# Kernel tuning notes

Hardware: AMD Instinct MI355X
Metric: run time of the kernel (lower is better)

Reference implementation:

```python
import jax, jax.numpy as jnp
import numpy as np

H = 1024      # hidden_size
NH = 8        # num_attention_heads
HD = H // NH  # head dim = 128
FF = 3072     # DebertaConfig default intermediate_size
MAXPOS = 512  # max_position_embeddings
EPS = 1e-7    # DeBERTa layer_norm_eps


def layer_norm(x, g, b):
    m = jnp.mean(x, axis=-1, keepdims=True)
    v = jnp.mean((x - m) ** 2, axis=-1, keepdims=True)
    return (x - m) * jax.lax.rsqrt(v + EPS) * g + b


def setup_inputs() -> dict:
    key = jax.random.key(0)
    ks = jax.random.split(key, 12)
    s = 0.02  # init std
    B, S = 16, 512
    return {
        "x": jax.random.normal(ks[0], (B, S, H), jnp.float32),
        "pos_emb": jax.random.normal(ks[1], (MAXPOS, H), jnp.float32) * s,
        "emb_ln_g": jnp.ones((H,), jnp.float32),
        "emb_ln_b": jnp.zeros((H,), jnp.float32),
        "Wq": jax.random.normal(ks[2], (H, H), jnp.float32) * s,
        "Wk": jax.random.normal(ks[3], (H, H), jnp.float32) * s,
        "Wv": jax.random.normal(ks[4], (H, H), jnp.float32) * s,
        "q_bias": jax.random.normal(ks[5], (H,), jnp.float32) * s,
        "v_bias": jax.random.normal(ks[6], (H,), jnp.float32) * s,
        "Wo": jax.random.normal(ks[7], (H, H), jnp.float32) * s,
        "bo": jnp.zeros((H,), jnp.float32),
        "ln1_g": jnp.ones((H,), jnp.float32),
        "ln1_b": jnp.zeros((H,), jnp.float32),
        "Wi": jax.random.normal(ks[8], (H, FF), jnp.float32) * s,
        "bi": jnp.zeros((FF,), jnp.float32),
        "Wf": jax.random.normal(ks[9], (FF, H), jnp.float32) * s,
        "bf": jnp.zeros((H,), jnp.float32),
        "ln2_g": jnp.ones((H,), jnp.float32),
        "ln2_b": jnp.zeros((H,), jnp.float32),
    }


def reference(x, pos_emb, emb_ln_g, emb_ln_b, Wq, Wk, Wv, q_bias, v_bias,
              Wo, bo, ln1_g, ln1_b, Wi, bi, Wf, bf, ln2_g, ln2_b):
    B, S, _ = x.shape
    # DebertaEmbeddings: inputs_embeds + absolute position embeddings, LayerNorm (eval: no dropout)
    h = layer_norm(x + pos_emb[:S], emb_ln_g, emb_ln_b)
    # DisentangledSelfAttention with pos_att_type=[] -> standard attention, scale_factor=1;
    # in_proj has no bias, but q and v get learned bias vectors.
    q = (h @ Wq + q_bias).reshape(B, S, NH, HD).transpose(0, 2, 1, 3)  # [B,NH,S,HD]
    k = (h @ Wk).reshape(B, S, NH, HD).transpose(0, 2, 1, 3)
    v = (h @ Wv + v_bias).reshape(B, S, NH, HD).transpose(0, 2, 1, 3)
    scale = jnp.sqrt(jnp.asarray(HD, x.dtype))
    scores = jnp.einsum('bhqd,bhkd->bhqk', q / scale, k)  # [B,NH,S,S]
    probs = jax.nn.softmax(scores, axis=-1)  # attention_mask all ones -> plain softmax
    ctx = jnp.einsum('bhqk,bhkd->bhqd', probs, v)
    ctx = ctx.transpose(0, 2, 1, 3).reshape(B, S, H)
    # SelfOutput: dense + residual + LayerNorm
    attn_out = layer_norm(ctx @ Wo + bo + h, ln1_g, ln1_b)
    # Intermediate (exact gelu) + Output: dense + residual + LayerNorm
    ff = jax.nn.gelu(attn_out @ Wi + bi, approximate=False)
    out = layer_norm(ff @ Wf + bf + attn_out, ln2_g, ln2_b)
    return out
```

## Files before the change

kernel.cpp:

```cpp
#include <hip/hip_runtime.h>
#include <hip/hip_bf16.h>

#define BB  16
#define SS  512
#define HH  1024
#define NHH 8
#define HDD 128
#define FFF 3072
#define TT  (BB * SS)

typedef __hip_bfloat16 bf16;
typedef short s8v __attribute__((ext_vector_type(8)));
typedef float f4v __attribute__((ext_vector_type(4)));

__device__ __forceinline__ float bf2f(bf16 v) { return __bfloat162float(v); }
__device__ __forceinline__ bf16 f2bf(float f) { return __float2bfloat16(f); }
__device__ __forceinline__ float us2f(unsigned short u) {
  union { unsigned int i; float f; } c; c.i = (unsigned int)u << 16; return c.f;
}

__global__ void embed_ln_kernel(const float* __restrict__ x, const float* __restrict__ pos,
                                const float* __restrict__ g, const float* __restrict__ bta,
                                bf16* __restrict__ h) {
  int t = blockIdx.x;
  int s = t & (SS - 1);
  int tid = threadIdx.x;
  const float* xr = x + (size_t)t * HH;
  const float* pr = pos + (size_t)s * HH;
  float vals[4];
  float sum = 0.f;
#pragma unroll
  for (int i = 0; i < 4; i++) {
    int c = tid + i * 256;
    vals[i] = xr[c] + pr[c];
    sum += vals[i];
  }
  __shared__ float red[4];
#pragma unroll
  for (int off = 32; off > 0; off >>= 1) sum += __shfl_down(sum, off, 64);
  if ((tid & 63) == 0) red[tid >> 6] = sum;
  __syncthreads();
  float mean = (red[0] + red[1] + red[2] + red[3]) * (1.f / HH);
  float vsum = 0.f;
#pragma unroll
  for (int i = 0; i < 4; i++) { float d = vals[i] - mean; vsum += d * d; }
  __syncthreads();
#pragma unroll
  for (int off = 32; off > 0; off >>= 1) vsum += __shfl_down(vsum, off, 64);
  if ((tid & 63) == 0) red[tid >> 6] = vsum;
  __syncthreads();
  float rstd = rsqrtf((red[0] + red[1] + red[2] + red[3]) * (1.f / HH) + 1e-7f);
  bf16* hr = h + (size_t)t * HH;
#pragma unroll
  for (int i = 0; i < 4; i++) {
    int c = tid + i * 256;
    hr[c] = f2bf((vals[i] - mean) * rstd * g[c] + bta[c]);
  }
}

template <int OUT_F32>
__global__ void add_ln_kernel(const bf16* __restrict__ a, const bf16* __restrict__ res,
                              const float* __restrict__ g, const float* __restrict__ bta,
                              void* __restrict__ outv) {
  int t = blockIdx.x;
  int tid = threadIdx.x;
  const bf16* ar = a + (size_t)t * HH;
  const bf16* rr = res + (size_t)t * HH;
  float vals[4];
  float sum = 0.f;
#pragma unroll
  for (int i = 0; i < 4; i++) {
    int c = tid + i * 256;
    vals[i] = bf2f(ar[c]) + bf2f(rr[c]);
    sum += vals[i];
  }
  __shared__ float red[4];
#pragma unroll
  for (int off = 32; off > 0; off >>= 1) sum += __shfl_down(sum, off, 64);
  if ((tid & 63) == 0) red[tid >> 6] = sum;
  __syncthreads();
  float mean = (red[0] + red[1] + red[2] + red[3]) * (1.f / HH);
  float vsum = 0.f;
#pragma unroll
  for (int i = 0; i < 4; i++) { float d = vals[i] - mean; vsum += d * d; }
  __syncthreads();
#pragma unroll
  for (int off = 32; off > 0; off >>= 1) vsum += __shfl_down(vsum, off, 64);
  if ((tid & 63) == 0) red[tid >> 6] = vsum;
  __syncthreads();
  float rstd = rsqrtf((red[0] + red[1] + red[2] + red[3]) * (1.f / HH) + 1e-7f);
#pragma unroll
  for (int i = 0; i < 4; i++) {
    int c = tid + i * 256;
    float o = (vals[i] - mean) * rstd * g[c] + bta[c];
    if (OUT_F32)
      ((float*)outv)[(size_t)t * HH + c] = o;
    else
      ((bf16*)outv)[(size_t)t * HH + c] = f2bf(o);
  }
}

__global__ void convert_w_kernel(const float* __restrict__ W, bf16* __restrict__ Wt,
                                 int K, int N) {
  __shared__ float tile[32][33];
  int n0 = blockIdx.x * 32, k0 = blockIdx.y * 32;
#pragma unroll
  for (int it = 0; it < 4; it++) {
    int idx = threadIdx.x + it * 256;
    int ty = idx >> 5, tx = idx & 31;
    tile[ty][tx] = W[(size_t)(k0 + ty) * N + n0 + tx];
  }
  __syncthreads();
#pragma unroll
  for (int it = 0; it < 4; it++) {
    int idx = threadIdx.x + it * 256;
    int ty = idx >> 5, tx = idx & 31;
    Wt[(size_t)(n0 + ty) * K + k0 + tx] = f2bf(tile[tx][ty]);
  }
}

__global__ void build_qkv_bias_kernel(const float* __restrict__ qb,
                                      const float* __restrict__ vb,
                                      float* __restrict__ o) {
  int i = blockIdx.x * 256 + threadIdx.x;
  float v = 0.f;
  if (i < HH) v = qb[i];
  else if (i >= 2 * HH) v = vb[i - 2 * HH];
  o[i] = v;
}

__global__ void transpose_v_kernel(const bf16* __restrict__ v, bf16* __restrict__ vt) {
  __shared__ unsigned short tile[32][33];
  int bh = blockIdx.z;
  int s0 = blockIdx.x * 32, d0 = blockIdx.y * 32;
  int b = bh >> 3, hd = bh & 7;
  const unsigned short* vp = (const unsigned short*)v + ((size_t)b * SS) * (3 * HH) + hd * HDD;
  unsigned short* vtp = (unsigned short*)vt + (size_t)bh * HDD * SS;
#pragma unroll
  for (int it = 0; it < 4; it++) {
    int idx = threadIdx.x + it * 256;
    int ty = idx >> 5, tx = idx & 31;
    tile[ty][tx] = vp[(size_t)(s0 + ty) * (3 * HH) + d0 + tx];
  }
  __syncthreads();
#pragma unroll
  for (int it = 0; it < 4; it++) {
    int idx = threadIdx.x + it * 256;
    int ty = idx >> 5, tx = idx & 31;
    vtp[(size_t)(d0 + ty) * SS + s0 + tx] = tile[tx][ty];
  }
}

template <int GELU>
__global__ __launch_bounds__(256)
void mfma_gemm_kernel(const bf16* __restrict__ A, int lda, long long sAb, long long sAh,
                      const bf16* __restrict__ Bt, int ldb, long long sBb, long long sBh,
                      const float* __restrict__ bias,
                      bf16* __restrict__ C, int ldc, long long sCb, long long sCh,
                      int M, int N, int K, float scale) {
  __shared__ unsigned short Als[128 * 40];
  __shared__ unsigned short Bls[128 * 40];
  int tid = threadIdx.x;
  int lane = tid & 63, wave = tid >> 6;
  int l15 = lane & 15, quad = lane >> 4;
  int wm = wave & 1, wn = wave >> 1;
  int m0 = blockIdx.y * 128, n0 = blockIdx.x * 128;
  int zb = blockIdx.z >> 3, zh = blockIdx.z & 7;
  const bf16* Ab = A + zb * sAb + zh * sAh;
  const bf16* Bb = Bt + zb * sBb + zh * sBh;
  bf16* Cb = C + zb * sCb + zh * sCh;
  f4v acc[4][4];
#pragma unroll
  for (int i = 0; i < 4; i++)
#pragma unroll
    for (int j = 0; j < 4; j++) acc[i][j] = (f4v){0.f, 0.f, 0.f, 0.f};
  int r0 = tid >> 2;
  int q8 = (tid & 3) * 8;
  const bf16* Ap0 = Ab + (size_t)(m0 + r0) * lda + q8;
  const bf16* Ap1 = Ab + (size_t)(m0 + r0 + 64) * lda + q8;
  const bf16* Bp0 = Bb + (size_t)(n0 + r0) * ldb + q8;
  const bf16* Bp1 = Bb + (size_t)(n0 + r0 + 64) * ldb + q8;
  uint4 a0 = *(const uint4*)(Ap0);
  uint4 a1 = *(const uint4*)(Ap1);
  uint4 b0 = *(const uint4*)(Bp0);
  uint4 b1 = *(const uint4*)(Bp1);
  for (int k0 = 0; k0 < K; k0 += 32) {
    *(uint4*)&Als[r0 * 40 + q8] = a0;
    *(uint4*)&Als[(r0 + 64) * 40 + q8] = a1;
    *(uint4*)&Bls[r0 * 40 + q8] = b0;
    *(uint4*)&Bls[(r0 + 64) * 40 + q8] = b1;
    __syncthreads();
    int kn = k0 + 32;
    if (kn < K) {
      a0 = *(const uint4*)(Ap0 + kn);
      a1 = *(const uint4*)(Ap1 + kn);
      b0 = *(const uint4*)(Bp0 + kn);
      b1 = *(const uint4*)(Bp1 + kn);
    }
    s8v af[4], bfr[4];
#pragma unroll
    for (int i = 0; i < 4; i++)
      af[i] = *(const s8v*)&Als[(wm * 64 + i * 16 + l15) * 40 + quad * 8];
#pragma unroll
    for (int j = 0; j < 4; j++)
      bfr[j] = *(const s8v*)&Bls[(wn * 64 + j * 16 + l15) * 40 + quad * 8];
#pragma unroll
    for (int i = 0; i < 4; i++)
#pragma unroll
      for (int j = 0; j < 4; j++)
        acc[i][j] = __builtin_amdgcn_mfma_f32_16x16x32_bf16(af[i], bfr[j], acc[i][j], 0, 0, 0);
    __syncthreads();
  }
#pragma unroll
  for (int i = 0; i < 4; i++) {
#pragma unroll
    for (int j = 0; j < 4; j++) {
      int n = n0 + wn * 64 + j * 16 + l15;
      float bval = bias ? bias[n] : 0.f;
#pragma unroll
      for (int r = 0; r < 4; r++) {
        int m = m0 + wm * 64 + i * 16 + quad * 4 + r;
        float v = (acc[i][j][r] + bval) * scale;
        if (GELU) v = 0.5f * v * (1.f + erff(v * 0.70710678118654752f));
        Cb[(size_t)m * ldc + n] = f2bf(v);
      }
    }
  }
}

__global__ void softmax_kernel(bf16* __restrict__ sc) {
  int wave = threadIdx.x >> 6, lane = threadIdx.x & 63;
  size_t row = (size_t)blockIdx.x * 4 + wave;
  unsigned short* p = (unsigned short*)sc + row * SS + lane * 8;
  union { uint4 u4; unsigned short u[8]; } buf;
  buf.u4 = *(const uint4*)p;
  float v[8];
  float mx = -1e30f;
#pragma unroll
  for (int j = 0; j < 8; j++) { v[j] = us2f(buf.u[j]); mx = fmaxf(mx, v[j]); }
#pragma unroll
  for (int off = 32; off > 0; off >>= 1) mx = fmaxf(mx, __shfl_xor(mx, off));
  float sum = 0.f;
#pragma unroll
  for (int j = 0; j < 8; j++) { v[j] = __expf(v[j] - mx); sum += v[j]; }
#pragma unroll
  for (int off = 32; off > 0; off >>= 1) sum += __shfl_xor(sum, off);
  float inv = 1.f / sum;
  union { uint4 u4; unsigned short u[8]; } obuf;
#pragma unroll
  for (int j = 0; j < 8; j++) {
    bf16 b = f2bf(v[j] * inv);
    obuf.u[j] = *(unsigned short*)&b;
  }
  *(uint4*)p = obuf.u4;
}

extern "C" void kernel_launch(void* const* d_in, const int* in_sizes, int n_in,
                              void* d_out, int out_size, void* d_ws, size_t ws_size,
                              hipStream_t stream) {
  const float* x     = (const float*)d_in[0];
  const float* pos   = (const float*)d_in[1];
  const float* eg    = (const float*)d_in[2];
  const float* ebeta = (const float*)d_in[3];
  const float* Wq    = (const float*)d_in[4];
  const float* Wk    = (const float*)d_in[5];
  const float* Wv    = (const float*)d_in[6];
  const float* qbias = (const float*)d_in[7];
  const float* vbias = (const float*)d_in[8];
  const float* Wo    = (const float*)d_in[9];
  const float* bo    = (const float*)d_in[10];
  const float* l1g   = (const float*)d_in[11];
  const float* l1b   = (const float*)d_in[12];
  const float* Wi    = (const float*)d_in[13];
  const float* bi    = (const float*)d_in[14];
  const float* Wf    = (const float*)d_in[15];
  const float* bfb   = (const float*)d_in[16];
  const float* l2g   = (const float*)d_in[17];
  const float* l2b   = (const float*)d_in[18];

  char* w = (char*)d_ws;
  const size_t MB = (size_t)1 << 20;
  bf16* h      = (bf16*)(w + 0 * MB);
  bf16* qkv    = (bf16*)(w + 16 * MB);
  bf16* ctx    = (bf16*)(w + 64 * MB);
  bf16* tmp1   = (bf16*)(w + 80 * MB);
  bf16* attn   = (bf16*)(w + 96 * MB);
  bf16* scores = (bf16*)(w + 112 * MB);
  bf16* ff     = (bf16*)(w + 112 * MB);
  bf16* tmp2   = (bf16*)(w + 176 * MB);
  bf16* vt     = (bf16*)(w + 192 * MB);
  bf16* Wqkvt  = (bf16*)(w + 208 * MB);
  bf16* Wot    = (bf16*)(w + 214 * MB);
  bf16* Wit    = (bf16*)(w + 216 * MB);
  bf16* Wft    = (bf16*)(w + 222 * MB);
  float* qkvb  = (float*)(w + 228 * MB);
  float* out   = (float*)d_out;

  const float QSCALE = 0.08838834764831845f;

  embed_ln_kernel<<<TT, 256, 0, stream>>>(x, pos, eg, ebeta, h);

  convert_w_kernel<<<dim3(HH / 32, HH / 32), 256, 0, stream>>>(Wq, Wqkvt, HH, HH);
  convert_w_kernel<<<dim3(HH / 32, HH / 32), 256, 0, stream>>>(Wk, Wqkvt + (size_t)HH * HH, HH, HH);
  convert_w_kernel<<<dim3(HH / 32, HH / 32), 256, 0, stream>>>(Wv, Wqkvt + (size_t)2 * HH * HH, HH, HH);
  convert_w_kernel<<<dim3(HH / 32, HH / 32), 256, 0, stream>>>(Wo, Wot, HH, HH);
  convert_w_kernel<<<dim3(FFF / 32, HH / 32), 256, 0, stream>>>(Wi, Wit, HH, FFF);
  convert_w_kernel<<<dim3(HH / 32, FFF / 32), 256, 0, stream>>>(Wf, Wft, FFF, HH);
  build_qkv_bias_kernel<<<12, 256, 0, stream>>>(qbias, vbias, qkvb);

  mfma_gemm_kernel<0><<<dim3(24, 64, 1), 256, 0, stream>>>(
      h, HH, 0, 0, Wqkvt, HH, 0, 0, qkvb, qkv, 3 * HH, 0, 0, TT, 3 * HH, HH, 1.f);

  mfma_gemm_kernel<0><<<dim3(4, 4, BB * NHH), 256, 0, stream>>>(
      qkv, 3 * HH, (long long)SS * 3 * HH, HDD,
      qkv + HH, 3 * HH, (long long)SS * 3 * HH, HDD,
      nullptr,
      scores, SS, (long long)NHH * SS * SS, (long long)SS * SS,
      SS, SS, HDD, QSCALE);

  softmax_kernel<<<BB * NHH * SS / 4, 256, 0, stream>>>(scores);

  transpose_v_kernel<<<dim3(SS / 32, HDD / 32, BB * NHH), 256, 0, stream>>>(qkv + 2 * HH, vt);

  mfma_gemm_kernel<0><<<dim3(1, 4, BB * NHH), 256, 0, stream>>>(
      scores, SS, (long long)NHH * SS * SS, (long long)SS * SS,
      vt, SS, (long long)NHH * HDD * SS, (long long)HDD * SS,
      nullptr,
      ctx, HH, (long long)SS * HH, HDD,
      SS, HDD, SS, 1.f);

  mfma_gemm_kernel<0><<<dim3(8, 64, 1), 256, 0, stream>>>(
      ctx, HH, 0, 0, Wot, HH, 0, 0, bo, tmp1, HH, 0, 0, TT, HH, HH, 1.f);
  add_ln_kernel<0><<<TT, 256, 0, stream>>>(tmp1, h, l1g, l1b, attn);

  mfma_gemm_kernel<1><<<dim3(24, 64, 1), 256, 0, stream>>>(
      attn, HH, 0, 0, Wit, HH, 0, 0, bi, ff, FFF, 0, 0, TT, FFF, HH, 1.f);
  mfma_gemm_kernel<0><<<dim3(8, 64, 1), 256, 0, stream>>>(
      ff, FFF, 0, 0, Wft, FFF, 0, 0, bfb, tmp2, HH, 0, 0, TT, HH, FFF, 1.f);
  add_ln_kernel<1><<<TT, 256, 0, stream>>>(tmp2, attn, l2g, l2b, out);
}
```

Measured before the change: 531.8 us.

## Add 256x256-tile MFMA GEMM with direct global-to-LDS staging for dense projections

Introduces a new 512-thread GEMM kernel using 256x256 output tiles, double-buffered LDS filled via global_load_lds with XOR-swizzled layout, interleaved with 16x16x32 bf16 MFMAs under raised wave priority. It replaces the previous 128x128-style GEMM for the QKV, output, intermediate and final FFN projections. The aim is higher arithmetic intensity per block and overlap of global loads with MFMA work. In exchange it uses 128KB LDS per block and many registers, which limits occupancy, and it relies on hand-placed barriers and vmcnt waits whose correctness depends on exact load counts.

```diff
diff --git a/kernel.cpp b/kernel.cpp
--- a/kernel.cpp
+++ b/kernel.cpp
@@ -228,6 +228,177 @@
   }
 }
 
+#define G256_BAR() asm volatile("s_barrier" ::: "memory")
+
+__device__ __forceinline__ void g256_stage_half(
+    const bf16* __restrict__ base, int ldx, int tile, int half,
+    unsigned op_byte, unsigned short* lds, int trow, int tcol8, int wave) {
+  const bf16* g0 = base + (size_t)(half * 128 + trow) * ldx + tile * 64 + tcol8;
+  const bf16* g1 = g0 + (size_t)64 * ldx;
+  unsigned off = op_byte + (unsigned)(tile & 1) * 32768u + (unsigned)half * 16384u +
+                 (unsigned)wave * 1024u;
+  unsigned l0 = (unsigned)(size_t)((char*)lds + off);
+  unsigned l1 = l0 + 8192u;
+  __builtin_amdgcn_global_load_lds(
+      (const __attribute__((address_space(1))) void*)(size_t)g0,
+      (__attribute__((address_space(3))) unsigned int*)l0, 16, 0, 0);
+  __builtin_amdgcn_global_load_lds(
+      (const __attribute__((address_space(1))) void*)(size_t)g1,
+      (__attribute__((address_space(3))) unsigned int*)l1, 16, 0, 0);
+}
+
+__device__ __forceinline__ void g256_read_a(
+    const unsigned short* lds, int buf, int sel, int wm, int l15, int quad,
+    s8v out[4][2]) {
+  int xr = l15 & 7;
+#pragma unroll
+  for (int i = 0; i < 4; i++) {
+    int R = wm * 128 + sel * 64 + i * 16 + l15;
+#pragma unroll
+    for (int kk = 0; kk < 2; kk++) {
+      int ch = (kk * 4 + quad) ^ xr;
+      out[i][kk] = *(const s8v*)&lds[buf * 16384 + R * 64 + ch * 8];
+    }
+  }
+}
+
+__device__ __forceinline__ void g256_read_b(
+    const unsigned short* lds, int buf, int sel, int wn, int l15, int quad,
+    s8v out[2][2]) {
+  int xr = l15 & 7;
+#pragma unroll
+  for (int j = 0; j < 2; j++) {
+    int R = wn * 64 + sel * 32 + j * 16 + l15;
+#pragma unroll
+    for (int kk = 0; kk < 2; kk++) {
+      int ch = (kk * 4 + quad) ^ xr;
+      out[j][kk] = *(const s8v*)&lds[32768 + buf * 16384 + R * 64 + ch * 8];
+    }
+  }
+}
+
+__device__ __forceinline__ void g256_mfma_quad(
+    const s8v a[4][2], const s8v b[2][2], f4v acc[8][4], int ag, int bg) {
+  __builtin_amdgcn_s_setprio(1);
+#pragma unroll
+  for (int i = 0; i < 4; i++)
+#pragma unroll
+    for (int j = 0; j < 2; j++)
+#pragma unroll
+      for (int kk = 0; kk < 2; kk++)
+        acc[ag * 4 + i][bg * 2 + j] = __builtin_amdgcn_mfma_f32_16x16x32_bf16(
+            a[i][kk], b[j][kk], acc[ag * 4 + i][bg * 2 + j], 0, 0, 0);
+  __builtin_amdgcn_s_setprio(0);
+}
+
+template <int GELU>
+__global__ __launch_bounds__(512, 2)
+void gemm256_kernel(const bf16* __restrict__ A, int lda,
+                    const bf16* __restrict__ Bt, int ldb,
+                    const float* __restrict__ bias,
+                    bf16* __restrict__ C, int ldc,
+                    int M, int N, int K) {
+  __shared__ __align__(128) unsigned short lds[65536];
+  int tid = threadIdx.x;
+  int lane = tid & 63, wave = tid >> 6;
+  int l15 = lane & 15, quad = lane >> 4;
+  int wm = wave >> 2, wn = wave & 3;
+  int m0 = blockIdx.y * 256, n0 = blockIdx.x * 256;
+  int trow = tid >> 3;
+  int tcol8 = ((tid & 7) ^ ((tid >> 3) & 7)) * 8;
+  const bf16* Ag = A + (size_t)m0 * lda;
+  const bf16* Bg = Bt + (size_t)n0 * ldb;
+
+  f4v acc[8][4];
+#pragma unroll
+  for (int i = 0; i < 8; i++)
+#pragma unroll
+    for (int j = 0; j < 4; j++) acc[i][j] = (f4v){0.f, 0.f, 0.f, 0.f};
+
+  g256_stage_half(Ag, lda, 0, 0, 0, lds, trow, tcol8, wave);
+  g256_stage_half(Ag, lda, 0, 1, 0, lds, trow, tcol8, wave);
+  g256_stage_half(Bg, ldb, 0, 0, 65536, lds, trow, tcol8, wave);
+  g256_stage_half(Bg, ldb, 0, 1, 65536, lds, trow, tcol8, wave);
+  g256_stage_half(Ag, lda, 1, 0, 0, lds, trow, tcol8, wave);
+  g256_stage_half(Ag, lda, 1, 1, 0, lds, trow, tcol8, wave);
+  g256_stage_half(Bg, ldb, 1, 0, 65536, lds, trow, tcol8, wave);
+  asm volatile("s_waitcnt vmcnt(6)" ::: "memory");
+  G256_BAR();
+
+  int niter = K >> 7;
+  for (int it = 0; it < niter; ++it) {
+    int t = it * 2;
+    bool more = (it < niter - 1);
+    s8v a0[4][2], a1[4][2], b0f[2][2], b1f[2][2];
+    g256_read_a(lds, 0, 0, wm, l15, quad, a0);
+    g256_read_b(lds, 0, 0, wn, l15, quad, b0f);
+    g256_stage_half(Bg, ldb, t + 1, 1, 65536, lds, trow, tcol8, wave);
+    G256_BAR();
+    g256_mfma_quad(a0, b0f, acc, 0, 0);
+    G256_BAR();
+    g256_read_a(lds, 0, 1, wm, l15, quad, a1);
+    g256_read_b(lds, 0, 1, wn, l15, quad, b1f);
+    G256_BAR();
+    g256_mfma_quad(a1, b0f, acc, 1, 0);
+    G256_BAR();
+    if (more) {
+      g256_stage_half(Ag, lda, t + 2, 0, 0, lds, trow, tcol8, wave);
+      g256_stage_half(Ag, lda, t + 2, 1, 0, lds, trow, tcol8, wave);
+    }
+    G256_BAR();
+    g256_mfma_quad(a1, b1f, acc, 1, 1);
+    G256_BAR();
+    if (more) g256_stage_half(Bg, ldb, t + 2, 0, 65536, lds, trow, tcol8, wave);
+    G256_BAR();
+    g256_mfma_quad(a0, b1f, acc, 0, 1);
+    if (more) { asm volatile("s_waitcnt vmcnt(6)" ::: "memory"); }
+    else      { asm volatile("s_waitcnt vmcnt(0)" ::: "memory"); }
+    G256_BAR();
+    g256_read_a(lds, 1, 0, wm, l15, quad, a0);
+    g256_read_b(lds, 1, 0, wn, l15, quad, b0f);
+    if (more) g256_stage_half(Bg, ldb, t + 2, 1, 65536, lds, trow, tcol8, wave);
+    G256_BAR();
+    g256_mfma_quad(a0, b0f, acc, 0, 0);
+    G256_BAR();
+    g256_read_a(lds, 1, 1, wm, l15, quad, a1);
+    g256_read_b(lds, 1, 1, wn, l15, quad, b1f);
+    G256_BAR();
+    g256_mfma_quad(a1, b0f, acc, 1, 0);
+    G256_BAR();
+    if (more) {
+      g256_stage_half(Ag, lda, t + 3, 0, 0, lds, trow, tcol8, wave);
+      g256_stage_half(Ag, lda, t + 3, 1, 0, lds, trow, tcol8, wave);
+    }
+    G256_BAR();
+    g256_mfma_quad(a1, b1f, acc, 1, 1);
+    G256_BAR();
+    if (more) g256_stage_half(Bg, ldb, t + 3, 0, 65536, lds, trow, tcol8, wave);
+    G256_BAR();
+    g256_mfma_quad(a0, b1f, acc, 0, 1);
+    if (more) asm volatile("s_waitcnt vmcnt(6)" ::: "memory");
+    G256_BAR();
+  }
+
+#pragma unroll
+  for (int sa = 0; sa < 2; sa++)
+#pragma unroll
+    for (int i = 0; i < 4; i++)
+#pragma unroll
+      for (int sb = 0; sb < 2; sb++)
+#pragma unroll
+        for (int j = 0; j < 2; j++) {
+          int n = n0 + wn * 64 + sb * 32 + j * 16 + l15;
+          float bval = bias[n];
+#pragma unroll
+          for (int r = 0; r < 4; r++) {
+            int m = m0 + wm * 128 + sa * 64 + i * 16 + quad * 4 + r;
+            float v = acc[sa * 4 + i][sb * 2 + j][r] + bval;
+            if (GELU) v = 0.5f * v * (1.f + erff(v * 0.70710678118654752f));
+            C[(size_t)m * ldc + n] = f2bf(v);
+          }
+        }
+}
+
 __global__ void softmax_kernel(bf16* __restrict__ sc) {
   int wave = threadIdx.x >> 6, lane = threadIdx.x & 63;
   size_t row = (size_t)blockIdx.x * 4 + wave;
@@ -308,8 +479,8 @@
   convert_w_kernel<<<dim3(HH / 32, FFF / 32), 256, 0, stream>>>(Wf, Wft, FFF, HH);
   build_qkv_bias_kernel<<<12, 256, 0, stream>>>(qbias, vbias, qkvb);
 
-  mfma_gemm_kernel<0><<<dim3(24, 64, 1), 256, 0, stream>>>(
-      h, HH, 0, 0, Wqkvt, HH, 0, 0, qkvb, qkv, 3 * HH, 0, 0, TT, 3 * HH, HH, 1.f);
+  gemm256_kernel<0><<<dim3(12, 32), 512, 0, stream>>>(
+      h, HH, Wqkvt, HH, qkvb, qkv, 3 * HH, TT, 3 * HH, HH);
 
   mfma_gemm_kernel<0><<<dim3(4, 4, BB * NHH), 256, 0, stream>>>(
       qkv, 3 * HH, (long long)SS * 3 * HH, HDD,
@@ -329,13 +500,13 @@
       ctx, HH, (long long)SS * HH, HDD,
       SS, HDD, SS, 1.f);
 
-  mfma_gemm_kernel<0><<<dim3(8, 64, 1), 256, 0, stream>>>(
-      ctx, HH, 0, 0, Wot, HH, 0, 0, bo, tmp1, HH, 0, 0, TT, HH, HH, 1.f);
+  gemm256_kernel<0><<<dim3(4, 32), 512, 0, stream>>>(
+      ctx, HH, Wot, HH, bo, tmp1, HH, TT, HH, HH);
   add_ln_kernel<0><<<TT, 256, 0, stream>>>(tmp1, h, l1g, l1b, attn);
 
-  mfma_gemm_kernel<1><<<dim3(24, 64, 1), 256, 0, stream>>>(
-      attn, HH, 0, 0, Wit, HH, 0, 0, bi, ff, FFF, 0, 0, TT, FFF, HH, 1.f);
-  mfma_gemm_kernel<0><<<dim3(8, 64, 1), 256, 0, stream>>>(
-      ff, FFF, 0, 0, Wft, FFF, 0, 0, bfb, tmp2, HH, 0, 0, TT, HH, FFF, 1.f);
+  gemm256_kernel<1><<<dim3(12, 32), 512, 0, stream>>>(
+      attn, HH, Wit, HH, bi, ff, FFF, TT, FFF, HH);
+  gemm256_kernel<0><<<dim3(4, 32), 512, 0, stream>>>(
+      ff, FFF, Wft, FFF, bfb, tmp2, HH, TT, HH, FFF);
   add_ln_kernel<1><<<TT, 256, 0, stream>>>(tmp2, attn, l2g, l2b, out);
 }
```

Result: slower. 694.1 us (+30.5%).

## Load GEMM tiles directly into LDS with XOR-swizzled layout

Applied to the files above, without the earlier changes.

The MFMA GEMM now copies A and B tiles straight from global memory into LDS using global_load_lds, instead of going through registers. The LDS tile shrinks from padded rows of 40 to unpadded rows of 32. An XOR swizzle on the 8-element column chunks is meant to avoid bank conflicts on the fragment reads. This frees the registers used for staging, but it drops the register prefetch of the next K slice, so global load latency is no longer overlapped with the MFMA work inside a block.

```diff
diff --git a/kernel.cpp b/kernel.cpp
--- a/kernel.cpp
+++ b/kernel.cpp
@@ -158,8 +158,8 @@
                       const float* __restrict__ bias,
                       bf16* __restrict__ C, int ldc, long long sCb, long long sCh,
                       int M, int N, int K, float scale) {
-  __shared__ unsigned short Als[128 * 40];
-  __shared__ unsigned short Bls[128 * 40];
+  __shared__ __align__(16) unsigned short Als[128 * 32];
+  __shared__ __align__(16) unsigned short Bls[128 * 32];
   int tid = threadIdx.x;
   int lane = tid & 63, wave = tid >> 6;
   int l15 = lane & 15, quad = lane >> 4;
@@ -174,36 +174,43 @@
   for (int i = 0; i < 4; i++)
 #pragma unroll
     for (int j = 0; j < 4; j++) acc[i][j] = (f4v){0.f, 0.f, 0.f, 0.f};
-  int r0 = tid >> 2;
-  int q8 = (tid & 3) * 8;
-  const bf16* Ap0 = Ab + (size_t)(m0 + r0) * lda + q8;
-  const bf16* Ap1 = Ab + (size_t)(m0 + r0 + 64) * lda + q8;
-  const bf16* Bp0 = Bb + (size_t)(n0 + r0) * ldb + q8;
-  const bf16* Bp1 = Bb + (size_t)(n0 + r0 + 64) * ldb + q8;
-  uint4 a0 = *(const uint4*)(Ap0);
-  uint4 a1 = *(const uint4*)(Ap1);
-  uint4 b0 = *(const uint4*)(Bp0);
-  uint4 b1 = *(const uint4*)(Bp1);
+
+  int srow = tid >> 2;
+  int scol = ((tid & 3) ^ (srow & 3)) * 8;
+  const bf16* ApLo = Ab + (size_t)(m0 + srow) * lda + scol;
+  const bf16* ApHi = Ab + (size_t)(m0 + srow + 64) * lda + scol;
+  const bf16* BpLo = Bb + (size_t)(n0 + srow) * ldb + scol;
+  const bf16* BpHi = Bb + (size_t)(n0 + srow + 64) * ldb + scol;
+  unsigned lA0 = (unsigned)(size_t)(Als + tid * 8);
+  unsigned lA1 = (unsigned)(size_t)(Als + 2048 + tid * 8);
+  unsigned lB0 = (unsigned)(size_t)(Bls + tid * 8);
+  unsigned lB1 = (unsigned)(size_t)(Bls + 2048 + tid * 8);
+
   for (int k0 = 0; k0 < K; k0 += 32) {
-    *(uint4*)&Als[r0 * 40 + q8] = a0;
-    *(uint4*)&Als[(r0 + 64) * 40 + q8] = a1;
-    *(uint4*)&Bls[r0 * 40 + q8] = b0;
-    *(uint4*)&Bls[(r0 + 64) * 40 + q8] = b1;
+    __builtin_amdgcn_global_load_lds(
+        (const __attribute__((address_space(1))) void*)(ApLo + k0),
+        (__attribute__((address_space(3))) unsigned int*)(size_t)lA0, 16, 0, 0);
+    __builtin_amdgcn_global_load_lds(
+        (const __attribute__((address_space(1))) void*)(ApHi + k0),
+        (__attribute__((address_space(3))) unsigned int*)(size_t)lA1, 16, 0, 0);
+    __builtin_amdgcn_global_load_lds(
+        (const __attribute__((address_space(1))) void*)(BpLo + k0),
+        (__attribute__((address_space(3))) unsigned int*)(size_t)lB0, 16, 0, 0);
+    __builtin_amdgcn_global_load_lds(
+        (const __attribute__((address_space(1))) void*)(BpHi + k0),
+        (__attribute__((address_space(3))) unsigned int*)(size_t)lB1, 16, 0, 0);
     __syncthreads();
-    int kn = k0 + 32;
-    if (kn < K) {
-      a0 = *(const uint4*)(Ap0 + kn);
-      a1 = *(const uint4*)(Ap1 + kn);
-      b0 = *(const uint4*)(Bp0 + kn);
-      b1 = *(const uint4*)(Bp1 + kn);
+    s8v af[4], bfr[4];
+#pragma unroll
+    for (int i = 0; i < 4; i++) {
+      int R = wm * 64 + i * 16 + l15;
+      af[i] = *(const s8v*)&Als[R * 32 + ((quad ^ (R & 3)) * 8)];
     }
-    s8v af[4], bfr[4];
-#pragma unroll
-    for (int i = 0; i < 4; i++)
-      af[i] = *(const s8v*)&Als[(wm * 64 + i * 16 + l15) * 40 + quad * 8];
-#pragma unroll
-    for (int j = 0; j < 4; j++)
-      bfr[j] = *(const s8v*)&Bls[(wn * 64 + j * 16 + l15) * 40 + quad * 8];
+#pragma unroll
+    for (int j = 0; j < 4; j++) {
+      int R = wn * 64 + j * 16 + l15;
+      bfr[j] = *(const s8v*)&Bls[R * 32 + ((quad ^ (R & 3)) * 8)];
+    }
 #pragma unroll
     for (int i = 0; i < 4; i++)
 #pragma unroll
```

After: 566.2 us. +6.5%, slower.

## Swizzle GEMM LDS layout and add double-buffered direct-to-LDS GEMM for FFN up-projection

Applied to the files above, without the earlier changes.

Replaces the padded 40-element LDS row stride with a 32-element stride plus an XOR swizzle on the 16-byte chunk index, which avoids bank conflicts while using less shared memory in every GEMM. It also adds a new GEMM kernel for the GELU intermediate projection. That kernel uses global_load_lds to stream tiles straight into double-buffered LDS, so the next tile's loads overlap the current tile's MFMAs. In exchange the code depends on the LDS-direct load semantics and the XOR layout matching the per-lane write ordering, and it relies on only one barrier per iteration for correctness.

```diff
diff --git a/kernel.cpp b/kernel.cpp
--- a/kernel.cpp
+++ b/kernel.cpp
@@ -158,8 +158,8 @@
                       const float* __restrict__ bias,
                       bf16* __restrict__ C, int ldc, long long sCb, long long sCh,
                       int M, int N, int K, float scale) {
-  __shared__ unsigned short Als[128 * 40];
-  __shared__ unsigned short Bls[128 * 40];
+  __shared__ __align__(16) unsigned short Als[128 * 32];
+  __shared__ __align__(16) unsigned short Bls[128 * 32];
   int tid = threadIdx.x;
   int lane = tid & 63, wave = tid >> 6;
   int l15 = lane & 15, quad = lane >> 4;
@@ -176,6 +176,10 @@
     for (int j = 0; j < 4; j++) acc[i][j] = (f4v){0.f, 0.f, 0.f, 0.f};
   int r0 = tid >> 2;
   int q8 = (tid & 3) * 8;
+  int fw = (r0 >> 1) & 3;
+  int wlo = r0 * 32 + (((tid & 3) ^ fw) * 8);
+  int whi = (r0 + 64) * 32 + (((tid & 3) ^ fw) * 8);
+  int qx = (quad ^ ((l15 >> 1) & 3)) * 8;
   const bf16* Ap0 = Ab + (size_t)(m0 + r0) * lda + q8;
   const bf16* Ap1 = Ab + (size_t)(m0 + r0 + 64) * lda + q8;
   const bf16* Bp0 = Bb + (size_t)(n0 + r0) * ldb + q8;
@@ -185,10 +189,10 @@
   uint4 b0 = *(const uint4*)(Bp0);
   uint4 b1 = *(const uint4*)(Bp1);
   for (int k0 = 0; k0 < K; k0 += 32) {
-    *(uint4*)&Als[r0 * 40 + q8] = a0;
-    *(uint4*)&Als[(r0 + 64) * 40 + q8] = a1;
-    *(uint4*)&Bls[r0 * 40 + q8] = b0;
-    *(uint4*)&Bls[(r0 + 64) * 40 + q8] = b1;
+    *(uint4*)&Als[wlo] = a0;
+    *(uint4*)&Als[whi] = a1;
+    *(uint4*)&Bls[wlo] = b0;
+    *(uint4*)&Bls[whi] = b1;
     __syncthreads();
     int kn = k0 + 32;
     if (kn < K) {
@@ -200,10 +204,10 @@
     s8v af[4], bfr[4];
 #pragma unroll
     for (int i = 0; i < 4; i++)
-      af[i] = *(const s8v*)&Als[(wm * 64 + i * 16 + l15) * 40 + quad * 8];
+      af[i] = *(const s8v*)&Als[(wm * 64 + i * 16 + l15) * 32 + qx];
 #pragma unroll
     for (int j = 0; j < 4; j++)
-      bfr[j] = *(const s8v*)&Bls[(wn * 64 + j * 16 + l15) * 40 + quad * 8];
+      bfr[j] = *(const s8v*)&Bls[(wn * 64 + j * 16 + l15) * 32 + qx];
 #pragma unroll
     for (int i = 0; i < 4; i++)
 #pragma unroll
@@ -223,6 +227,90 @@
         float v = (acc[i][j][r] + bval) * scale;
         if (GELU) v = 0.5f * v * (1.f + erff(v * 0.70710678118654752f));
         Cb[(size_t)m * ldc + n] = f2bf(v);
+      }
+    }
+  }
+}
+
+template <int GELU>
+__global__ __launch_bounds__(256)
+void gemm_dbuf_kernel(const bf16* __restrict__ A, int lda,
+                      const bf16* __restrict__ Bt, int ldb,
+                      const float* __restrict__ bias,
+                      bf16* __restrict__ C, int ldc,
+                      int M, int N, int K, float scale) {
+  __shared__ __align__(16) unsigned short As2[2 * 128 * 32];
+  __shared__ __align__(16) unsigned short Bs2[2 * 128 * 32];
+  int tid = threadIdx.x;
+  int lane = tid & 63, wave = tid >> 6;
+  int l15 = lane & 15, quad = lane >> 4;
+  int wm = wave & 1, wn = wave >> 1;
+  int m0 = blockIdx.y * 128, n0 = blockIdx.x * 128;
+  f4v acc[4][4];
+#pragma unroll
+  for (int i = 0; i < 4; i++)
+#pragma unroll
+    for (int j = 0; j < 4; j++) acc[i][j] = (f4v){0.f, 0.f, 0.f, 0.f};
+  int srow = tid >> 2;
+  int scol = (((tid & 3) ^ ((tid >> 3) & 3))) * 8;
+  const bf16* ApLo = A + (size_t)(m0 + srow) * lda + scol;
+  const bf16* ApHi = A + (size_t)(m0 + srow + 64) * lda + scol;
+  const bf16* BpLo = Bt + (size_t)(n0 + srow) * ldb + scol;
+  const bf16* BpHi = Bt + (size_t)(n0 + srow + 64) * ldb + scol;
+  int qx = (quad ^ ((l15 >> 1) & 3)) * 8;
+  int niter = K >> 5;
+
+#define V2_STAGE(kk, buf) do {                                                  \
+    unsigned _o = (unsigned)(buf) * 4096u + (unsigned)tid * 8u;                 \
+    __builtin_amdgcn_global_load_lds(                                           \
+        (const __attribute__((address_space(1))) void*)(ApLo + (kk)),           \
+        (__attribute__((address_space(3))) unsigned int*)(size_t)               \
+            (unsigned)(size_t)(As2 + _o), 16, 0, 0);                            \
+    __builtin_amdgcn_global_load_lds(                                           \
+        (const __attribute__((address_space(1))) void*)(ApHi + (kk)),           \
+        (__attribute__((address_space(3))) unsigned int*)(size_t)               \
+            (unsigned)(size_t)(As2 + _o + 2048u), 16, 0, 0);                    \
+    __builtin_amdgcn_global_load_lds(                                           \
+        (const __attribute__((address_space(1))) void*)(BpLo + (kk)),           \
+        (__attribute__((address_space(3))) unsigned int*)(size_t)               \
+            (unsigned)(size_t)(Bs2 + _o), 16, 0, 0);                            \
+    __builtin_amdgcn_global_load_lds(                                           \
+        (const __attribute__((address_space(1))) void*)(BpHi + (kk)),           \
+        (__attribute__((address_space(3))) unsigned int*)(size_t)               \
+            (unsigned)(size_t)(Bs2 + _o + 2048u), 16, 0, 0);                    \
+  } while (0)
+
+  V2_STAGE(0, 0);
+  for (int it = 0; it < niter; ++it) {
+    __syncthreads();
+    if (it + 1 < niter) V2_STAGE((it + 1) * 32, (it + 1) & 1);
+    int buf = it & 1;
+    s8v af[4], bfr[4];
+#pragma unroll
+    for (int i = 0; i < 4; i++)
+      af[i] = *(const s8v*)&As2[buf * 4096 + (wm * 64 + i * 16 + l15) * 32 + qx];
+#pragma unroll
+    for (int j = 0; j < 4; j++)
+      bfr[j] = *(const s8v*)&Bs2[buf * 4096 + (wn * 64 + j * 16 + l15) * 32 + qx];
+#pragma unroll
+    for (int i = 0; i < 4; i++)
+#pragma unroll
+      for (int j = 0; j < 4; j++)
+        acc[i][j] = __builtin_amdgcn_mfma_f32_16x16x32_bf16(af[i], bfr[j], acc[i][j], 0, 0, 0);
+  }
+#undef V2_STAGE
+#pragma unroll
+  for (int i = 0; i < 4; i++) {
+#pragma unroll
+    for (int j = 0; j < 4; j++) {
+      int n = n0 + wn * 64 + j * 16 + l15;
+      float bval = bias ? bias[n] : 0.f;
+#pragma unroll
+      for (int r = 0; r < 4; r++) {
+        int m = m0 + wm * 64 + i * 16 + quad * 4 + r;
+        float v = (acc[i][j][r] + bval) * scale;
+        if (GELU) v = 0.5f * v * (1.f + erff(v * 0.70710678118654752f));
+        C[(size_t)m * ldc + n] = f2bf(v);
       }
     }
   }
@@ -333,8 +421,8 @@
       ctx, HH, 0, 0, Wot, HH, 0, 0, bo, tmp1, HH, 0, 0, TT, HH, HH, 1.f);
   add_ln_kernel<0><<<TT, 256, 0, stream>>>(tmp1, h, l1g, l1b, attn);
 
-  mfma_gemm_kernel<1><<<dim3(24, 64, 1), 256, 0, stream>>>(
-      attn, HH, 0, 0, Wit, HH, 0, 0, bi, ff, FFF, 0, 0, TT, FFF, HH, 1.f);
+  gemm_dbuf_kernel<1><<<dim3(24, 64, 1), 256, 0, stream>>>(
+      attn, HH, Wit, HH, bi, ff, FFF, TT, FFF, HH, 1.f);
   mfma_gemm_kernel<0><<<dim3(8, 64, 1), 256, 0, stream>>>(
       ff, FFF, 0, 0, Wft, FFF, 0, 0, bfb, tmp2, HH, 0, 0, TT, HH, FFF, 1.f);
   add_ln_kernel<1><<<TT, 256, 0, stream>>>(tmp2, attn, l2g, l2b, out);
```

After: 529.3 us. About the same (-0.5%).
